# Kernel optimization log

Hardware: AMD Instinct MI355X
Metric: run time of the kernel (lower is better)

Reference implementation:

```python
import jax, jax.numpy as jnp
import numpy as np


def _cosine_alpha_bar(T, s=0.008):
    x = np.linspace(0.0, T, T + 1)
    ac = np.cos((x / T + s) / (1.0 + s) * np.pi / 2.0) ** 2
    ac = ac / ac[0]
    betas = np.clip(1.0 - ac[1:] / ac[:-1], 1e-5, 0.999)
    return jnp.asarray(np.cumprod(1.0 - betas), dtype=jnp.float32)


def setup_inputs():
    B, T, C, D, L, NS = 16, 1024, 16, 256, 4, 1000
    ks = list(jax.random.split(jax.random.key(0), 64))
    def w(i, shape, fan):
        return jax.random.normal(ks[i], shape, dtype=jnp.float32) / np.sqrt(fan)
    half = D // 2
    nf = half // 2
    inp = {}
    inp['x'] = jax.random.normal(ks[0], (B, T, C), dtype=jnp.float32)
    inp['t'] = jax.random.randint(ks[1], (B,), 0, NS, dtype=jnp.int32)
    dt = jax.random.uniform(ks[2], (B, T), minval=5e-4, maxval=2e-3, dtype=jnp.float32)
    inp['timestamps'] = jnp.cumsum(dt, axis=1)
    inp['mask'] = (jax.random.uniform(ks[3], (B, T, C)) > 0.3).astype(jnp.float32)
    inp['noise'] = jax.random.normal(ks[4], (B, T, D), dtype=jnp.float32)
    inp['n_heads'] = 4
    inp['alpha_bar'] = _cosine_alpha_bar(NS)
    inp['W_enc'] = w(5, (2 * C, D), 2 * C); inp['b_enc'] = jnp.zeros((D,), jnp.float32)
    inp['te_freqs'] = jnp.exp(-jnp.arange(half, dtype=jnp.float32) * np.log(10000.0) / half)
    inp['W_temb'] = w(6, (D, D), D); inp['b_temb'] = jnp.zeros((D,), jnp.float32)
    inp['th_a'] = 0.1 * jax.random.normal(ks[7], (half,), dtype=jnp.float32)
    inp['th_b'] = 0.1 * jax.random.normal(ks[8], (half,), dtype=jnp.float32)
    inp['th_freqs'] = (jnp.exp(-jnp.linspace(0.0, np.log(10000.0 / 4.0), nf)) * (2.0 * np.pi / 4.0)).astype(jnp.float32)
    inp['W_film'] = w(9, (D, 2 * D), D); inp['b_film'] = jnp.zeros((2 * D,), jnp.float32)
    inp['gru_Wih'] = w(10, (D, 3 * D), D); inp['gru_Whh'] = w(11, (D, 3 * D), D)
    inp['gru_bih'] = jnp.zeros((3 * D,), jnp.float32); inp['gru_bhh'] = jnp.zeros((3 * D,), jnp.float32)
    inp['ode_W1'] = w(12, (D, D), D); inp['ode_b1'] = jnp.zeros((D,), jnp.float32)
    inp['ode_W2'] = w(13, (D, D), D); inp['ode_b2'] = jnp.zeros((D,), jnp.float32)
    inp['tr_Wqkv'] = w(14, (L, D, 3 * D), D); inp['tr_bqkv'] = jnp.zeros((L, 3 * D), jnp.float32)
    inp['tr_Wo'] = w(15, (L, D, D), D); inp['tr_bo'] = jnp.zeros((L, D), jnp.float32)
    inp['tr_ln1_w'] = jnp.ones((L, D), jnp.float32); inp['tr_ln1_b'] = jnp.zeros((L, D), jnp.float32)
    inp['tr_ln2_w'] = jnp.ones((L, D), jnp.float32); inp['tr_ln2_b'] = jnp.zeros((L, D), jnp.float32)
    inp['tr_W1'] = w(16, (L, D, 4 * D), D); inp['tr_b1'] = jnp.zeros((L, 4 * D), jnp.float32)
    inp['tr_W2'] = w(17, (L, 4 * D, D), 4 * D); inp['tr_b2'] = jnp.zeros((L, D), jnp.float32)
    inp['trn_w'] = jnp.ones((D,), jnp.float32); inp['trn_b'] = jnp.zeros((D,), jnp.float32)
    return inp


def _ln(u, w_, b_):
    m = u.mean(-1, keepdims=True)
    v = u.var(-1, keepdims=True)
    return (u - m) / jnp.sqrt(v + 1e-5) * w_ + b_


def reference(x, t, timestamps, mask, noise, n_heads, alpha_bar, W_enc, b_enc, te_freqs, W_temb, b_temb, th_a, th_b, th_freqs, W_film, b_film, gru_Wih, gru_Whh, gru_bih, gru_bhh, ode_W1, ode_b1, ode_W2, ode_b2, tr_Wqkv, tr_bqkv, tr_Wo, tr_bo, tr_ln1_w, tr_ln1_b, tr_ln2_w, tr_ln2_b, tr_W1, tr_b1, tr_W2, tr_b2, trn_w, trn_b):
    B, T, C = x.shape
    D = W_enc.shape[1]
    hd = D // n_heads
    # latent encode + forward diffusion
    z = jax.nn.relu(jnp.concatenate([x, mask], -1) @ W_enc + b_enc)  # (B,T,D)
    ab = alpha_bar[t][:, None, None]
    h = jnp.sqrt(ab) * z + jnp.sqrt(1.0 - ab) * noise
    # diffusion-step sinusoidal embedding
    targ = t.astype(jnp.float32)[:, None] * te_freqs[None, :]
    te = (jnp.concatenate([jnp.sin(targ), jnp.cos(targ)], -1) @ W_temb + b_temb)[:, None, :]
    # TimeHybridEncoding: odd dims ramp, even dims interleaved sin/cos
    ts = timestamps
    ramp = ts[..., None] * th_a + th_b                       # (B,T,D/2)
    phase = ts[..., None] * th_freqs                         # (B,T,D/4)
    sc = jnp.stack([jnp.sin(phase), jnp.cos(phase)], -1).reshape(B, T, -1)
    tm = jnp.zeros((B, T, D), x.dtype).at[..., 0::2].set(sc).at[..., 1::2].set(ramp)
    gamma, beta = jnp.split(jax.nn.silu(te) @ W_film + b_film, 2, -1)
    tm = (1.0 + gamma) * tm + beta
    h = h + te + tm
    # Jump-ODE encoder: RK4 between events + GRUCell jump, as a scan
    dts = jnp.concatenate([jnp.zeros((B, 1), x.dtype), ts[:, 1:] - ts[:, :-1]], 1)[..., None]  # (B,T,1); dt0=0 -> identity ODE step
    def odef(hh):
        return jnp.tanh(hh @ ode_W1 + ode_b1) @ ode_W2 + ode_b2
    def step(hh, inp):
        xt, dt = inp
        f1 = odef(hh)
        f2 = odef(hh + 0.5 * dt * f1)
        f3 = odef(hh + 0.5 * dt * f2)
        f4 = odef(hh + dt * f3)
        hh = hh + dt / 6.0 * (f1 + 2.0 * f2 + 2.0 * f3 + f4)
        gi = xt @ gru_Wih + gru_bih
        gh = hh @ gru_Whh + gru_bhh
        ir, iz, inn = jnp.split(gi, 3, -1)
        hr, hz, hn = jnp.split(gh, 3, -1)
        r = jax.nn.sigmoid(ir + hr)
        zg = jax.nn.sigmoid(iz + hz)
        n = jnp.tanh(inn + r * hn)
        hh = (1.0 - zg) * n + zg * hh
        return hh, hh
    _, Hs = jax.lax.scan(step, jnp.zeros((B, D), x.dtype), (jnp.swapaxes(h, 0, 1), jnp.swapaxes(dts, 0, 1)))
    Hseq = jnp.swapaxes(Hs, 0, 1)  # (B,T,D)
    # pre-norm causal transformer encoder (eval mode, relu FFN), final LayerNorm
    causal = jnp.triu(jnp.full((T, T), -jnp.inf, dtype=x.dtype), 1)
    Ht = Hseq
    for l in range(tr_Wqkv.shape[0]):
        u = _ln(Ht, tr_ln1_w[l], tr_ln1_b[l])
        q, k, v = jnp.split(u @ tr_Wqkv[l] + tr_bqkv[l], 3, -1)
        q = q.reshape(B, T, n_heads, hd).transpose(0, 2, 1, 3)
        k = k.reshape(B, T, n_heads, hd).transpose(0, 2, 1, 3)
        v = v.reshape(B, T, n_heads, hd).transpose(0, 2, 1, 3)
        att = jax.nn.softmax(jnp.einsum('bhqd,bhkd->bhqk', q, k) / np.sqrt(hd) + causal, axis=-1)
        o = jnp.einsum('bhqk,bhkd->bhqd', att, v).transpose(0, 2, 1, 3).reshape(B, T, D)
        Ht = Ht + o @ tr_Wo[l] + tr_bo[l]
        u2 = _ln(Ht, tr_ln2_w[l], tr_ln2_b[l])
        Ht = Ht + jax.nn.relu(u2 @ tr_W1[l] + tr_b1[l]) @ tr_W2[l] + tr_b2[l]
    Ht = _ln(Ht, trn_w, trn_b)
    return Hseq + Ht
```

## Files before the change

### kernel.cpp

```cpp
#include <hip/hip_runtime.h>

#define Bz  16
#define Tz  1024
#define Cz  16
#define Dz  256
#define NHz 4
#define HDz 64
#define Lz  4
#define MROWS (Bz*Tz)
#define QB  8

__device__ __forceinline__ float sigmoidf_(float x){ return 1.0f/(1.0f+__expf(-x)); }
__device__ __forceinline__ float tanh_(float x){
  float e = __expf(2.f*x);
  return 1.f - 2.f/(e + 1.f);
}

__device__ __forceinline__ float dot2f(uint a, uint b, float c){
  float d;
  asm("v_dot2_f32_f16 %0, %1, %2, %3" : "=v"(d) : "v"(a), "v"(b), "v"(c));
  return d;
}
__device__ __forceinline__ uint f2h2(float a, float b){
  union { _Float16 h[2]; uint u; } r;
  r.h[0] = (_Float16)a; r.h[1] = (_Float16)b;
  return r.u;
}

__device__ __forceinline__ float red8(float a){
  int x = __builtin_amdgcn_update_dpp(0, __float_as_int(a), 0xB1, 0xF, 0xF, true);
  a += __int_as_float(x);
  x = __builtin_amdgcn_update_dpp(0, __float_as_int(a), 0x4E, 0xF, 0xF, true);
  a += __int_as_float(x);
  a += __shfl_xor(a, 4);
  return a;
}

__global__ __launch_bounds__(256) void k_prep(
    const float* __restrict__ W1, const float* __restrict__ W2, const float* __restrict__ Whh,
    uint* __restrict__ W1L, uint* __restrict__ W2L, uint* __restrict__ WhL)
{
  int m = blockIdx.x*256 + threadIdx.x;
  if (m < 65536){
    const float* W = (m < 32768) ? W1 : W2;
    uint* out = (m < 32768) ? W1L : W2L;
    int mm = m & 32767;
    int q = mm >> 2, cc = mm & 3;
    int i = q >> 9, l = q & 511;
    int j4 = l >> 3, ks = l & 7;
    int kp = ks*16 + i;
    int c = j4*4 + cc;
    out[mm] = f2h2(W[(2*kp)*256 + c], W[(2*kp+1)*256 + c]);
  } else if (m < 65536 + 98304){
    int mm = m - 65536;
    int g = mm >> 15;
    int r = mm & 32767;
    int q = r >> 2, cc = r & 3;
    int i = q >> 9, l = q & 511;
    int j4 = l >> 3, ks = l & 7;
    int kp = ks*16 + i;
    int c = j4*4 + cc;
    WhL[mm] = f2h2(Whh[(2*kp)*768 + g*256 + c], Whh[(2*kp+1)*768 + g*256 + c]);
  }
}

__global__ __launch_bounds__(256) void k_batch_emb(
    const int* __restrict__ t, const float* __restrict__ te_freqs,
    const float* __restrict__ W_temb, const float* __restrict__ b_temb,
    const float* __restrict__ W_film, const float* __restrict__ b_film,
    float* __restrict__ te_out, float* __restrict__ gamma_out, float* __restrict__ beta_out)
{
  int b = blockIdx.x; int j = threadIdx.x;
  __shared__ float s[256];
  __shared__ float ste[256];
  float tf = (float)t[b];
  if (j < 128){
    float targ = tf * te_freqs[j];
    s[j]     = __sinf(targ);
    s[j+128] = __cosf(targ);
  }
  __syncthreads();
  float a0=0,a1=0,a2=0,a3=0;
  #pragma unroll 8
  for (int k=0;k<256;k+=4){
    a0 = fmaf(s[k+0], W_temb[(k+0)*256+j], a0);
    a1 = fmaf(s[k+1], W_temb[(k+1)*256+j], a1);
    a2 = fmaf(s[k+2], W_temb[(k+2)*256+j], a2);
    a3 = fmaf(s[k+3], W_temb[(k+3)*256+j], a3);
  }
  float te = (a0+a1)+(a2+a3) + b_temb[j];
  te_out[b*256+j] = te;
  ste[j] = te * sigmoidf_(te);
  __syncthreads();
  float g0=0,g1=0,h0=0,h1=0;
  #pragma unroll 8
  for (int k=0;k<256;k+=2){
    float v0 = ste[k+0], v1 = ste[k+1];
    g0 = fmaf(v0, W_film[(k+0)*512+j],     g0);
    g1 = fmaf(v1, W_film[(k+1)*512+j],     g1);
    h0 = fmaf(v0, W_film[(k+0)*512+256+j], h0);
    h1 = fmaf(v1, W_film[(k+1)*512+256+j], h1);
  }
  gamma_out[b*256+j] = g0+g1 + b_film[j];
  beta_out [b*256+j] = h0+h1 + b_film[256+j];
}

__global__ __launch_bounds__(256) void k_encode(
    const float* __restrict__ x, const float* __restrict__ mask, const float* __restrict__ noise,
    const int* __restrict__ t, const float* __restrict__ alpha_bar, const float* __restrict__ ts,
    const float* __restrict__ W_enc, const float* __restrict__ b_enc,
    const float* __restrict__ th_a, const float* __restrict__ th_b, const float* __restrict__ th_freqs,
    const float* __restrict__ te, const float* __restrict__ gamma, const float* __restrict__ beta,
    float* __restrict__ H0)
{
  int bt = blockIdx.x; int b = bt >> 10;
  int j = threadIdx.x;
  __shared__ float in[32];
  if (j < 16)      in[j] = x[bt*16 + j];
  else if (j < 32) in[j] = mask[bt*16 + (j-16)];
  __syncthreads();
  float acc = 0.f;
  #pragma unroll
  for (int k=0;k<32;k++) acc = fmaf(in[k], W_enc[k*256+j], acc);
  float z = fmaxf(acc + b_enc[j], 0.f);
  float ab = alpha_bar[t[b]];
  float h = sqrtf(ab)*z + sqrtf(1.f-ab)*noise[(size_t)bt*256 + j];
  float tsv = ts[bt];
  float tm;
  if (j & 1){
    int i = (j-1) >> 1;
    tm = fmaf(tsv, th_a[i], th_b[i]);
  } else {
    int m = j >> 2;
    float ph = tsv * th_freqs[m];
    tm = ((j & 3) == 0) ? __sinf(ph) : __cosf(ph);
  }
  tm = fmaf(1.f + gamma[b*256+j], tm, beta[b*256+j]);
  H0[(size_t)bt*256 + j] = h + te[b*256+j] + tm;
}

template<bool RELU, bool RES>
__global__ __launch_bounds__(256) void k_gemm(
    const float* __restrict__ A, const float* __restrict__ W,
    const float* __restrict__ bias, const float* __restrict__ Rp,
    float* __restrict__ Cp, int M, int N, int K)
{
  __shared__ float As[16][68];
  __shared__ float Bs[16][64];
  int bn = blockIdx.x * 64, bm = blockIdx.y * 64;
  int tid = threadIdx.x;
  int tx = tid & 15, ty = tid >> 4;
  float acc[4][4] = {};
  for (int k0=0; k0<K; k0+=16){
    #pragma unroll
    for (int i=0;i<4;i++){
      int idx = tid + i*256;
      int m = idx >> 4, kk = idx & 15;
      As[kk][m] = A[(size_t)(bm+m)*K + k0+kk];
    }
    #pragma unroll
    for (int i=0;i<4;i++){
      int idx = tid + i*256;
      int kk = idx >> 6, n = idx & 63;
      Bs[kk][n] = W[(size_t)(k0+kk)*N + bn+n];
    }
    __syncthreads();
    #pragma unroll
    for (int kk=0;kk<16;kk++){
      float a0=As[kk][ty*4+0], a1=As[kk][ty*4+1], a2=As[kk][ty*4+2], a3=As[kk][ty*4+3];
      float b0=Bs[kk][tx*4+0], b1=Bs[kk][tx*4+1], b2=Bs[kk][tx*4+2], b3=Bs[kk][tx*4+3];
      acc[0][0]=fmaf(a0,b0,acc[0][0]); acc[0][1]=fmaf(a0,b1,acc[0][1]); acc[0][2]=fmaf(a0,b2,acc[0][2]); acc[0][3]=fmaf(a0,b3,acc[0][3]);
      acc[1][0]=fmaf(a1,b0,acc[1][0]); acc[1][1]=fmaf(a1,b1,acc[1][1]); acc[1][2]=fmaf(a1,b2,acc[1][2]); acc[1][3]=fmaf(a1,b3,acc[1][3]);
      acc[2][0]=fmaf(a2,b0,acc[2][0]); acc[2][1]=fmaf(a2,b1,acc[2][1]); acc[2][2]=fmaf(a2,b2,acc[2][2]); acc[2][3]=fmaf(a2,b3,acc[2][3]);
      acc[3][0]=fmaf(a3,b0,acc[3][0]); acc[3][1]=fmaf(a3,b1,acc[3][1]); acc[3][2]=fmaf(a3,b2,acc[3][2]); acc[3][3]=fmaf(a3,b3,acc[3][3]);
    }
    __syncthreads();
  }
  #pragma unroll
  for (int i=0;i<4;i++){
    int row = bm + ty*4 + i;
    #pragma unroll
    for (int jj=0;jj<4;jj++){
      int col = bn + tx*4 + jj;
      float v = acc[i][jj] + bias[col];
      if (RELU) v = fmaxf(v, 0.f);
      if (RES)  v += Rp[(size_t)row*N + col];
      Cp[(size_t)row*N + col] = v;
    }
  }
}

#define SCAN_LDS_BYTES (131072 + 1280)

#define DOT4V(WV, VW) { uint4 _w = (WV); \
  a0 = dot2f(_w.x, VW, a0); a1 = dot2f(_w.y, VW, a1); \
  a2 = dot2f(_w.z, VW, a2); a3 = dot2f(_w.w, VW, a3); }

#define MV16L(VB) { \
  uint4 q0=(VB)[ks5+0], q1=(VB)[ks5+1], q2=(VB)[ks5+2], q3=(VB)[ks5+3]; \
  DOT4V(w1s[0*512+tid], q0.x)  DOT4V(w1s[1*512+tid], q0.y)  DOT4V(w1s[2*512+tid], q0.z)  DOT4V(w1s[3*512+tid], q0.w)  \
  DOT4V(w1s[4*512+tid], q1.x)  DOT4V(w1s[5*512+tid], q1.y)  DOT4V(w1s[6*512+tid], q1.z)  DOT4V(w1s[7*512+tid], q1.w)  \
  DOT4V(w1s[8*512+tid], q2.x)  DOT4V(w1s[9*512+tid], q2.y)  DOT4V(w1s[10*512+tid], q2.z) DOT4V(w1s[11*512+tid], q2.w) \
  DOT4V(w1s[12*512+tid], q3.x) DOT4V(w1s[13*512+tid], q3.y) DOT4V(w1s[14*512+tid], q3.z) DOT4V(w1s[15*512+tid], q3.w) }

#define MV16R(W, VB) { \
  uint4 q0=(VB)[ks5+0], q1=(VB)[ks5+1], q2=(VB)[ks5+2], q3=(VB)[ks5+3]; \
  DOT4V(W[0], q0.x)  DOT4V(W[1], q0.y)  DOT4V(W[2], q0.z)  DOT4V(W[3], q0.w)  \
  DOT4V(W[4], q1.x)  DOT4V(W[5], q1.y)  DOT4V(W[6], q1.z)  DOT4V(W[7], q1.w)  \
  DOT4V(W[8], q2.x)  DOT4V(W[9], q2.y)  DOT4V(W[10], q2.z) DOT4V(W[11], q2.w) \
  DOT4V(W[12], q3.x) DOT4V(W[13], q3.y) DOT4V(W[14], q3.z) DOT4V(W[15], q3.w) }

#define DOTG(WV, VV, g0,g1,g2,g3) \
  g0 = dot2f((WV).x, VV, g0); g1 = dot2f((WV).y, VV, g1); \
  g2 = dot2f((WV).z, VV, g2); g3 = dot2f((WV).w, VV, g3);

#define LDQ(BUF, PO, I0) { \
  BUF[0]=WhL4[(PO)+((I0)+0)*512+tid]; BUF[1]=WhL4[(PO)+((I0)+1)*512+tid]; \
  BUF[2]=WhL4[(PO)+((I0)+2)*512+tid]; BUF[3]=WhL4[(PO)+((I0)+3)*512+tid]; }

#define DOTQ(BUF, Q, g0,g1,g2,g3) { \
  DOTG(BUF[0], (Q).x, g0,g1,g2,g3) DOTG(BUF[1], (Q).y, g0,g1,g2,g3) \
  DOTG(BUF[2], (Q).z, g0,g1,g2,g3) DOTG(BUF[3], (Q).w, g0,g1,g2,g3) }

__global__ __launch_bounds__(512, 2) void k_scan(
    const uint* __restrict__ W1Lg, const uint* __restrict__ W2Lg, const uint* __restrict__ WhLg,
    const float* __restrict__ GI, const float* __restrict__ ts,
    const float* __restrict__ b1, const float* __restrict__ b2,
    const float* __restrict__ bhh, float* __restrict__ Hseq, float* __restrict__ Ht)
{
  extern __shared__ __align__(16) char smem[];
  uint4* w1s = (uint4*)smem;
  uint*  v2  = (uint*)(smem + 131072);
  const int b = blockIdx.x, tid = threadIdx.x;
  const int j4 = tid >> 3, ks = tid & 7;
  const int ks5 = ks*5;
  const uint4* W1L4 = (const uint4*)W1Lg;
  const uint4* W2L4 = (const uint4*)W2Lg;
  const uint4* WhL4 = (const uint4*)WhLg;
  #pragma unroll
  for (int i=0;i<16;i++) w1s[i*512+tid] = W1L4[i*512+tid];
  uint4 w2r[16];
  #pragma unroll
  for (int i=0;i<16;i++) w2r[i] = W2L4[i*512 + tid];
  if (tid < 320) v2[tid] = 0u;
  const float4 b1v  = ((const float4*)b1)[j4];
  const float4 b2v  = ((const float4*)b2)[j4];
  const float4 bhrv = ((const float4*)bhh)[j4];
  const float4 bhzv = ((const float4*)bhh)[64 + j4];
  const float4 bhnv = ((const float4*)bhh)[128 + j4];
  const float* tsb = ts + b*Tz;
  const float* gib = GI + (size_t)b*Tz*768;
  float* hsq = Hseq + (size_t)b*Tz*256;
  float* htp = Ht   + (size_t)b*Tz*256;
  const int wdw = 2*j4;
  const int wslot = (wdw >> 4)*20 + (wdw & 15);
  float4 h = {0.f,0.f,0.f,0.f};
  float tprev = 0.f;
  int cur = 0;
  __syncthreads();

  for (int tt=0; tt<Tz; ++tt){
    float tcur = tsb[tt];
    float dt = tcur - tprev; if (tt == 0) dt = 0.f;
    tprev = tcur;
    uint* bufA = v2 + (cur ? 160 : 0);
    uint* bufB = v2 + (cur ? 0 : 160);
    const uint4* vbA = (const uint4*)bufA;
    const uint4* vbB = (const uint4*)bufB;
    uint4 wA[4], wB[4];

    {
      float a0=0,a1=0,a2=0,a3=0;
      MV16L(vbA);
      a0=red8(a0); a1=red8(a1); a2=red8(a2); a3=red8(a3);
      float u0 = tanh_(a0+b1v.x), u1 = tanh_(a1+b1v.y);
      float u2 = tanh_(a2+b1v.z), u3 = tanh_(a3+b1v.w);
      if (ks == 0){
        uint2 pk; pk.x = f2h2(u0,u1); pk.y = f2h2(u2,u3);
        *(uint2*)(bufB + wslot) = pk;
      }
    }
    __syncthreads();
    {
      float a0=0,a1=0,a2=0,a3=0;
      MV16R(w2r, vbB);
      a0=red8(a0); a1=red8(a1); a2=red8(a2); a3=red8(a3);
      float hm = 0.5f*dt;
      float m0 = fmaf(hm, a0+b2v.x, h.x);
      float m1 = fmaf(hm, a1+b2v.y, h.y);
      float m2 = fmaf(hm, a2+b2v.z, h.z);
      float m3 = fmaf(hm, a3+b2v.w, h.w);
      if (ks == 0){
        uint2 pk; pk.x = f2h2(m0,m1); pk.y = f2h2(m2,m3);
        *(uint2*)(bufA + wslot) = pk;
      }
    }
    __syncthreads();
    {
      float a0=0,a1=0,a2=0,a3=0;
      MV16L(vbA);
      a0=red8(a0); a1=red8(a1); a2=red8(a2); a3=red8(a3);
      float u0 = tanh_(a0+b1v.x), u1 = tanh_(a1+b1v.y);
      float u2 = tanh_(a2+b1v.z), u3 = tanh_(a3+b1v.w);
      if (ks == 0){
        uint2 pk; pk.x = f2h2(u0,u1); pk.y = f2h2(u2,u3);
        *(uint2*)(bufB + wslot) = pk;
      }
    }
    __syncthreads();
    float4 hn;
    const float4 gi_r = *(const float4*)(gib + tt*768       + j4*4);
    const float4 gi_z = *(const float4*)(gib + tt*768 + 256 + j4*4);
    const float4 gi_n = *(const float4*)(gib + tt*768 + 512 + j4*4);
    LDQ(wA, 0, 0)
    LDQ(wB, 0, 4)
    {
      float a0=0,a1=0,a2=0,a3=0;
      MV16R(w2r, vbB);
      a0=red8(a0); a1=red8(a1); a2=red8(a2); a3=red8(a3);
      hn.x = fmaf(dt, a0+b2v.x, h.x);
      hn.y = fmaf(dt, a1+b2v.y, h.y);
      hn.z = fmaf(dt, a2+b2v.z, h.z);
      hn.w = fmaf(dt, a3+b2v.w, h.w);
      if (ks == 0){
        uint2 pk; pk.x = f2h2(hn.x,hn.y); pk.y = f2h2(hn.z,hn.w);
        *(uint2*)(bufA + wslot) = pk;
      }
    }
    __syncthreads();
    {
      uint4 q0=vbA[ks5+0], q1=vbA[ks5+1], q2=vbA[ks5+2], q3=vbA[ks5+3];
      float r0=0,r1=0,r2=0,r3=0, z0=0,z1=0,z2=0,z3=0, n0=0,n1=0,n2=0,n3=0;
      DOTQ(wA, q0, r0,r1,r2,r3)  LDQ(wA, 0, 8)
      DOTQ(wB, q1, r0,r1,r2,r3)  LDQ(wB, 0, 12)
      DOTQ(wA, q2, r0,r1,r2,r3)  LDQ(wA, 8192, 0)
      DOTQ(wB, q3, r0,r1,r2,r3)  LDQ(wB, 8192, 4)
      DOTQ(wA, q0, z0,z1,z2,z3)  LDQ(wA, 8192, 8)
      DOTQ(wB, q1, z0,z1,z2,z3)  LDQ(wB, 8192, 12)
      DOTQ(wA, q2, z0,z1,z2,z3)  LDQ(wA, 16384, 0)
      DOTQ(wB, q3, z0,z1,z2,z3)  LDQ(wB, 16384, 4)
      DOTQ(wA, q0, n0,n1,n2,n3)  LDQ(wA, 16384, 8)
      DOTQ(wB, q1, n0,n1,n2,n3)  LDQ(wB, 16384, 12)
      DOTQ(wA, q2, n0,n1,n2,n3)
      DOTQ(wB, q3, n0,n1,n2,n3)
      r0=red8(r0); r1=red8(r1); r2=red8(r2); r3=red8(r3);
      z0=red8(z0); z1=red8(z1); z2=red8(z2); z3=red8(z3);
      n0=red8(n0); n1=red8(n1); n2=red8(n2); n3=red8(n3);
      float gr0 = sigmoidf_(gi_r.x + r0 + bhrv.x);
      float gr1 = sigmoidf_(gi_r.y + r1 + bhrv.y);
      float gr2 = sigmoidf_(gi_r.z + r2 + bhrv.z);
      float gr3 = sigmoidf_(gi_r.w + r3 + bhrv.w);
      float gz0 = sigmoidf_(gi_z.x + z0 + bhzv.x);
      float gz1 = sigmoidf_(gi_z.y + z1 + bhzv.y);
      float gz2 = sigmoidf_(gi_z.z + z2 + bhzv.z);
      float gz3 = sigmoidf_(gi_z.w + z3 + bhzv.w);
      float gn0 = tanh_(gi_n.x + gr0*(n0 + bhnv.x));
      float gn1 = tanh_(gi_n.y + gr1*(n1 + bhnv.y));
      float gn2 = tanh_(gi_n.z + gr2*(n2 + bhnv.z));
      float gn3 = tanh_(gi_n.w + gr3*(n3 + bhnv.w));
      h.x = fmaf(gz0, hn.x - gn0, gn0);
      h.y = fmaf(gz1, hn.y - gn1, gn1);
      h.z = fmaf(gz2, hn.z - gn2, gn2);
      h.w = fmaf(gz3, hn.w - gn3, gn3);
      if (ks == 0){
        uint2 pk; pk.x = f2h2(h.x,h.y); pk.y = f2h2(h.z,h.w);
        *(uint2*)(bufB + wslot) = pk;
        *(float4*)(hsq + tt*256 + j4*4) = h;
        *(float4*)(htp + tt*256 + j4*4) = h;
      }
    }
    cur ^= 1;
    __syncthreads();
  }
}

__global__ __launch_bounds__(256) void k_attn(const float* __restrict__ QKV, float* __restrict__ O)
{
  int qb = blockIdx.x & (Tz/QB - 1);
  int bh = blockIdx.x / (Tz/QB);
  int b = bh >> 2, h = bh & 3;
  __shared__ uint Q2[QB][32];
  __shared__ float S[QB][Tz];
  __shared__ __align__(16) char kvbuf[64*68*4];
  __shared__ float rs[QB];
  uint  (*K2)[33] = (uint(*)[33])kvbuf;
  float (*Vs)[68] = (float(*)[68])kvbuf;
  int tid = threadIdx.x;
  const float* base = QKV + (size_t)b*Tz*768;
  for (int i = tid; i < QB*16; i += 256){
    int q = i >> 4, c = i & 15;
    const float4 v = *(const float4*)&base[(size_t)(qb*QB+q)*768 + h*64 + c*4];
    Q2[q][c*2]   = f2h2(v.x*0.125f, v.y*0.125f);
    Q2[q][c*2+1] = f2h2(v.z*0.125f, v.w*0.125f);
  }
  __syncthreads();
  int kmax = qb*QB + QB;
  int nkt = (kmax + 63) >> 6;
  int q = tid >> 5, i0 = tid & 31;
  int qg = qb*QB + q;
  for (int kt=0; kt<nkt; ++kt){
    for (int i=tid; i<64*16; i+=256){
      int r=i>>4, c=i&15;
      const float4 v = *(const float4*)&base[(size_t)(kt*64+r)*768 + 256 + h*64 + c*4];
      K2[r][c*2]   = f2h2(v.x, v.y);
      K2[r][c*2+1] = f2h2(v.z, v.w);
    }
    __syncthreads();
    float a0=0.f, a1=0.f;
    #pragma unroll 8
    for (int dp=0; dp<32; ++dp){
      uint qv = Q2[q][dp];
      a0 = dot2f(K2[i0][dp],    qv, a0);
      a1 = dot2f(K2[i0+32][dp], qv, a1);
    }
    int k0g = kt*64 + i0, k1g = k0g + 32;
    S[q][kt*64+i0]    = (k0g <= qg) ? a0 : -1e30f;
    S[q][kt*64+i0+32] = (k1g <= qg) ? a1 : -1e30f;
    __syncthreads();
  }
  int NK = nkt*64;
  float m = -1e30f;
  for (int kk=i0; kk<NK; kk+=32) m = fmaxf(m, S[q][kk]);
  #pragma unroll
  for (int o=16;o;o>>=1) m = fmaxf(m, __shfl_xor(m, o, 32));
  float sum = 0.f;
  for (int kk=i0; kk<NK; kk+=32){
    float p = __expf(S[q][kk] - m);
    S[q][kk] = p;
    sum += p;
  }
  #pragma unroll
  for (int o=16;o;o>>=1) sum += __shfl_xor(sum, o, 32);
  if (i0 == 0) rs[q] = 1.f/sum;
  int dq = tid & 15;
  int ks = (tid >> 4) & 1;
  float o0=0,o1=0,o2=0,o3=0;
  for (int kt=0; kt<nkt; ++kt){
    __syncthreads();
    for (int i=tid; i<64*16; i+=256){
      int r=i>>4, c=i&15;
      const float4 v = *(const float4*)&base[(size_t)(kt*64+r)*768 + 512 + h*64 + c*4];
      *(float4*)&Vs[r][c*4] = v;
    }
    __syncthreads();
    int kbase = kt*64;
    #pragma unroll 8
    for (int kk=ks; kk<64; kk+=2){
      float p = S[q][kbase+kk];
      const float4 vv = *(const float4*)&Vs[kk][dq*4];
      o0=fmaf(p,vv.x,o0); o1=fmaf(p,vv.y,o1); o2=fmaf(p,vv.z,o2); o3=fmaf(p,vv.w,o3);
    }
  }
  o0 += __shfl_xor(o0, 16); o1 += __shfl_xor(o1, 16);
  o2 += __shfl_xor(o2, 16); o3 += __shfl_xor(o3, 16);
  if (!(tid & 16)){
    float r = rs[q];
    size_t orow = ((size_t)b*Tz + qg)*256 + h*64 + dq*4;
    float4 ov = {o0*r, o1*r, o2*r, o3*r};
    *(float4*)&O[orow] = ov;
  }
}

template<bool FINAL>
__global__ __launch_bounds__(256) void k_ln(
    const float* __restrict__ in, const float* __restrict__ w, const float* __restrict__ bgain,
    const float* __restrict__ addv, float* __restrict__ out)
{
  int row  = blockIdx.x*4 + (threadIdx.x >> 6);
  int lane = threadIdx.x & 63;
  const float4 xv = ((const float4*)(in + (size_t)row*256))[lane];
  float s = xv.x + xv.y + xv.z + xv.w;
  #pragma unroll
  for (int o=32;o;o>>=1) s += __shfl_xor(s, o, 64);
  float mean = s * (1.f/256.f);
  float dx=xv.x-mean, dy=xv.y-mean, dz=xv.z-mean, dw=xv.w-mean;
  float qv = dx*dx + dy*dy + dz*dz + dw*dw;
  #pragma unroll
  for (int o=32;o;o>>=1) qv += __shfl_xor(qv, o, 64);
  float rstd = 1.f/sqrtf(qv*(1.f/256.f) + 1e-5f);
  const float4 wv = ((const float4*)w)[lane];
  const float4 bv = ((const float4*)bgain)[lane];
  float4 ov;
  ov.x = dx*rstd*wv.x + bv.x;
  ov.y = dy*rstd*wv.y + bv.y;
  ov.z = dz*rstd*wv.z + bv.z;
  ov.w = dw*rstd*wv.w + bv.w;
  if (FINAL){
    const float4 av = ((const float4*)(addv + (size_t)row*256))[lane];
    ov.x += av.x; ov.y += av.y; ov.z += av.z; ov.w += av.w;
  }
  ((float4*)(out + (size_t)row*256))[lane] = ov;
}

extern "C" void kernel_launch(void* const* d_in, const int* in_sizes, int n_in,
                              void* d_out, int out_size, void* d_ws, size_t ws_size,
                              hipStream_t stream)
{
  const float* x         = (const float*)d_in[0];
  const int*   t         = (const int*)  d_in[1];
  const float* ts        = (const float*)d_in[2];
  const float* mask      = (const float*)d_in[3];
  const float* noise     = (const float*)d_in[4];
  const float* alpha_bar = (const float*)d_in[6];
  const float* W_enc     = (const float*)d_in[7];
  const float* b_enc     = (const float*)d_in[8];
  const float* te_freqs  = (const float*)d_in[9];
  const float* W_temb    = (const float*)d_in[10];
  const float* b_temb    = (const float*)d_in[11];
  const float* th_a      = (const float*)d_in[12];
  const float* th_b      = (const float*)d_in[13];
  const float* th_freqs  = (const float*)d_in[14];
  const float* W_film    = (const float*)d_in[15];
  const float* b_film    = (const float*)d_in[16];
  const float* gru_Wih   = (const float*)d_in[17];
  const float* gru_Whh   = (const float*)d_in[18];
  const float* gru_bih   = (const float*)d_in[19];
  const float* gru_bhh   = (const float*)d_in[20];
  const float* ode_W1    = (const float*)d_in[21];
  const float* ode_b1    = (const float*)d_in[22];
  const float* ode_W2    = (const float*)d_in[23];
  const float* ode_b2    = (const float*)d_in[24];
  const float* tr_Wqkv   = (const float*)d_in[25];
  const float* tr_bqkv   = (const float*)d_in[26];
  const float* tr_Wo     = (const float*)d_in[27];
  const float* tr_bo     = (const float*)d_in[28];
  const float* tr_ln1_w  = (const float*)d_in[29];
  const float* tr_ln1_b  = (const float*)d_in[30];
  const float* tr_ln2_w  = (const float*)d_in[31];
  const float* tr_ln2_b  = (const float*)d_in[32];
  const float* tr_W1     = (const float*)d_in[33];
  const float* tr_b1     = (const float*)d_in[34];
  const float* tr_W2     = (const float*)d_in[35];
  const float* tr_b2     = (const float*)d_in[36];
  const float* trn_w     = (const float*)d_in[37];
  const float* trn_b     = (const float*)d_in[38];

  float* w = (float*)d_ws;
  float* te    = w;
  float* gamma = w + 4096;
  float* beta  = w + 8192;
  float* R1    = w + 12288;
  float* H0    = R1;
  float* GI    = R1 + 4*1024*1024;
  float* QKVb  = R1;
  float* F1    = R1;
  float* Hseq  = R1   + 16*1024*1024;
  float* Ht    = Hseq + 4*1024*1024;
  float* U     = Ht   + 4*1024*1024;
  float* O     = U    + 4*1024*1024;
  uint*  W1L   = (uint*)(O + 4*1024*1024);
  uint*  W2L   = W1L + 32768;
  uint*  WhL   = W2L + 32768;

  k_prep<<<640, 256, 0, stream>>>(ode_W1, ode_W2, gru_Whh, W1L, W2L, WhL);
  k_batch_emb<<<Bz, 256, 0, stream>>>(t, te_freqs, W_temb, b_temb, W_film, b_film, te, gamma, beta);
  k_encode<<<MROWS, 256, 0, stream>>>(x, mask, noise, t, alpha_bar, ts, W_enc, b_enc,
                                      th_a, th_b, th_freqs, te, gamma, beta, H0);
  k_gemm<false,false><<<dim3(768/64, MROWS/64), 256, 0, stream>>>(H0, gru_Wih, gru_bih, nullptr, GI, MROWS, 768, 256);

  hipFuncSetAttribute((const void*)k_scan, hipFuncAttributeMaxDynamicSharedMemorySize, SCAN_LDS_BYTES);
  k_scan<<<Bz, 512, SCAN_LDS_BYTES, stream>>>(W1L, W2L, WhL, GI, ts, ode_b1, ode_b2, gru_bhh, Hseq, Ht);

  for (int l=0; l<Lz; ++l){
    k_ln<false><<<MROWS/4, 256, 0, stream>>>(Ht, tr_ln1_w + l*256, tr_ln1_b + l*256, nullptr, U);
    k_gemm<false,false><<<dim3(768/64, MROWS/64), 256, 0, stream>>>(U, tr_Wqkv + (size_t)l*256*768, tr_bqkv + l*768, nullptr, QKVb, MROWS, 768, 256);
    k_attn<<<Bz*NHz*(Tz/QB), 256, 0, stream>>>(QKVb, O);
    k_gemm<false,true><<<dim3(256/64, MROWS/64), 256, 0, stream>>>(O, tr_Wo + (size_t)l*256*256, tr_bo + l*256, Ht, Ht, MROWS, 256, 256);
    k_ln<false><<<MROWS/4, 256, 0, stream>>>(Ht, tr_ln2_w + l*256, tr_ln2_b + l*256, nullptr, U);
    k_gemm<true,false><<<dim3(1024/64, MROWS/64), 256, 0, stream>>>(U, tr_W1 + (size_t)l*256*1024, tr_b1 + l*1024, nullptr, F1, MROWS, 1024, 256);
    k_gemm<false,true><<<dim3(256/64, MROWS/64), 256, 0, stream>>>(F1, tr_W2 + (size_t)l*1024*256, tr_b2 + l*256, Ht, Ht, MROWS, 256, 1024);
  }

  k_ln<true><<<MROWS/4, 256, 0, stream>>>(Ht, trn_w, trn_b, Hseq, (float*)d_out);
}
```

Measured before the change: 12.93 ms.

## Double scan block to 1024 threads with 16-way K split per output

The sequential GRU/ODE scan kernel now runs 1024 threads per batch block instead of 512. Each group of four outputs is split across 16 K-slices rather than 8, which halves the per-thread dot-product chain, register weight footprint and global Whh loads per step. The weight prep layout, LDS vector padding and reductions (one more cross-lane shuffle) are adjusted to match. This trades shorter serial per-step latency for more reduction overhead and a larger synchronization domain at each barrier.

```diff
diff --git a/kernel.cpp b/kernel.cpp
--- a/kernel.cpp
+++ b/kernel.cpp
@@ -27,12 +27,13 @@
   return r.u;
 }
 
-__device__ __forceinline__ float red8(float a){
+__device__ __forceinline__ float red16(float a){
   int x = __builtin_amdgcn_update_dpp(0, __float_as_int(a), 0xB1, 0xF, 0xF, true);
   a += __int_as_float(x);
   x = __builtin_amdgcn_update_dpp(0, __float_as_int(a), 0x4E, 0xF, 0xF, true);
   a += __int_as_float(x);
   a += __shfl_xor(a, 4);
+  a += __shfl_xor(a, 8);
   return a;
 }
 
@@ -46,20 +47,20 @@
     uint* out = (m < 32768) ? W1L : W2L;
     int mm = m & 32767;
     int q = mm >> 2, cc = mm & 3;
-    int i = q >> 9, l = q & 511;
-    int j4 = l >> 3, ks = l & 7;
-    int kp = ks*16 + i;
-    int c = j4*4 + cc;
+    int i = q >> 10, l = q & 1023;
+    int ks = l & 15, j4g = l >> 4;
+    int kp = ks*8 + i;
+    int c = j4g*4 + cc;
     out[mm] = f2h2(W[(2*kp)*256 + c], W[(2*kp+1)*256 + c]);
   } else if (m < 65536 + 98304){
     int mm = m - 65536;
     int g = mm >> 15;
     int r = mm & 32767;
     int q = r >> 2, cc = r & 3;
-    int i = q >> 9, l = q & 511;
-    int j4 = l >> 3, ks = l & 7;
-    int kp = ks*16 + i;
-    int c = j4*4 + cc;
+    int i = q >> 10, l = q & 1023;
+    int ks = l & 15, j4g = l >> 4;
+    int kp = ks*8 + i;
+    int c = j4g*4 + cc;
     WhL[mm] = f2h2(Whh[(2*kp)*768 + g*256 + c], Whh[(2*kp+1)*768 + g*256 + c]);
   }
 }
@@ -190,39 +191,33 @@
   }
 }
 
-#define SCAN_LDS_BYTES (131072 + 1280)
+#define SCAN_LDS_BYTES (131072 + 1536)
 
 #define DOT4V(WV, VW) { uint4 _w = (WV); \
   a0 = dot2f(_w.x, VW, a0); a1 = dot2f(_w.y, VW, a1); \
   a2 = dot2f(_w.z, VW, a2); a3 = dot2f(_w.w, VW, a3); }
 
-#define MV16L(VB) { \
-  uint4 q0=(VB)[ks5+0], q1=(VB)[ks5+1], q2=(VB)[ks5+2], q3=(VB)[ks5+3]; \
-  DOT4V(w1s[0*512+tid], q0.x)  DOT4V(w1s[1*512+tid], q0.y)  DOT4V(w1s[2*512+tid], q0.z)  DOT4V(w1s[3*512+tid], q0.w)  \
-  DOT4V(w1s[4*512+tid], q1.x)  DOT4V(w1s[5*512+tid], q1.y)  DOT4V(w1s[6*512+tid], q1.z)  DOT4V(w1s[7*512+tid], q1.w)  \
-  DOT4V(w1s[8*512+tid], q2.x)  DOT4V(w1s[9*512+tid], q2.y)  DOT4V(w1s[10*512+tid], q2.z) DOT4V(w1s[11*512+tid], q2.w) \
-  DOT4V(w1s[12*512+tid], q3.x) DOT4V(w1s[13*512+tid], q3.y) DOT4V(w1s[14*512+tid], q3.z) DOT4V(w1s[15*512+tid], q3.w) }
-
-#define MV16R(W, VB) { \
-  uint4 q0=(VB)[ks5+0], q1=(VB)[ks5+1], q2=(VB)[ks5+2], q3=(VB)[ks5+3]; \
-  DOT4V(W[0], q0.x)  DOT4V(W[1], q0.y)  DOT4V(W[2], q0.z)  DOT4V(W[3], q0.w)  \
-  DOT4V(W[4], q1.x)  DOT4V(W[5], q1.y)  DOT4V(W[6], q1.z)  DOT4V(W[7], q1.w)  \
-  DOT4V(W[8], q2.x)  DOT4V(W[9], q2.y)  DOT4V(W[10], q2.z) DOT4V(W[11], q2.w) \
-  DOT4V(W[12], q3.x) DOT4V(W[13], q3.y) DOT4V(W[14], q3.z) DOT4V(W[15], q3.w) }
+#define MV8L(VB) { \
+  uint4 p0=(VB)[ks3+0], p1=(VB)[ks3+1]; \
+  DOT4V(w1s[0*1024+tid],p0.x) DOT4V(w1s[1*1024+tid],p0.y) \
+  DOT4V(w1s[2*1024+tid],p0.z) DOT4V(w1s[3*1024+tid],p0.w) \
+  DOT4V(w1s[4*1024+tid],p1.x) DOT4V(w1s[5*1024+tid],p1.y) \
+  DOT4V(w1s[6*1024+tid],p1.z) DOT4V(w1s[7*1024+tid],p1.w) }
+
+#define MV8R(W, VB) { \
+  uint4 p0=(VB)[ks3+0], p1=(VB)[ks3+1]; \
+  DOT4V(W[0],p0.x) DOT4V(W[1],p0.y) DOT4V(W[2],p0.z) DOT4V(W[3],p0.w) \
+  DOT4V(W[4],p1.x) DOT4V(W[5],p1.y) DOT4V(W[6],p1.z) DOT4V(W[7],p1.w) }
 
 #define DOTG(WV, VV, g0,g1,g2,g3) \
   g0 = dot2f((WV).x, VV, g0); g1 = dot2f((WV).y, VV, g1); \
   g2 = dot2f((WV).z, VV, g2); g3 = dot2f((WV).w, VV, g3);
 
-#define LDQ(BUF, PO, I0) { \
-  BUF[0]=WhL4[(PO)+((I0)+0)*512+tid]; BUF[1]=WhL4[(PO)+((I0)+1)*512+tid]; \
-  BUF[2]=WhL4[(PO)+((I0)+2)*512+tid]; BUF[3]=WhL4[(PO)+((I0)+3)*512+tid]; }
-
-#define DOTQ(BUF, Q, g0,g1,g2,g3) { \
-  DOTG(BUF[0], (Q).x, g0,g1,g2,g3) DOTG(BUF[1], (Q).y, g0,g1,g2,g3) \
-  DOTG(BUF[2], (Q).z, g0,g1,g2,g3) DOTG(BUF[3], (Q).w, g0,g1,g2,g3) }
-
-__global__ __launch_bounds__(512, 2) void k_scan(
+#define LDQ4(BUF, PO, I0) { \
+  BUF[0]=WhL4[(PO)+((I0)+0)*1024+tid]; BUF[1]=WhL4[(PO)+((I0)+1)*1024+tid]; \
+  BUF[2]=WhL4[(PO)+((I0)+2)*1024+tid]; BUF[3]=WhL4[(PO)+((I0)+3)*1024+tid]; }
+
+__global__ __launch_bounds__(1024, 4) void k_scan(
     const uint* __restrict__ W1Lg, const uint* __restrict__ W2Lg, const uint* __restrict__ WhLg,
     const float* __restrict__ GI, const float* __restrict__ ts,
     const float* __restrict__ b1, const float* __restrict__ b2,
@@ -232,17 +227,17 @@
   uint4* w1s = (uint4*)smem;
   uint*  v2  = (uint*)(smem + 131072);
   const int b = blockIdx.x, tid = threadIdx.x;
-  const int j4 = tid >> 3, ks = tid & 7;
-  const int ks5 = ks*5;
+  const int j4 = tid >> 4, ks = tid & 15;
+  const int ks3 = ks*3;
   const uint4* W1L4 = (const uint4*)W1Lg;
   const uint4* W2L4 = (const uint4*)W2Lg;
   const uint4* WhL4 = (const uint4*)WhLg;
   #pragma unroll
-  for (int i=0;i<16;i++) w1s[i*512+tid] = W1L4[i*512+tid];
-  uint4 w2r[16];
-  #pragma unroll
-  for (int i=0;i<16;i++) w2r[i] = W2L4[i*512 + tid];
-  if (tid < 320) v2[tid] = 0u;
+  for (int i=0;i<8;i++) w1s[i*1024+tid] = W1L4[i*1024+tid];
+  uint4 w2r[8];
+  #pragma unroll
+  for (int i=0;i<8;i++) w2r[i] = W2L4[i*1024 + tid];
+  if (tid < 384) v2[tid] = 0u;
   const float4 b1v  = ((const float4*)b1)[j4];
   const float4 b2v  = ((const float4*)b2)[j4];
   const float4 bhrv = ((const float4*)bhh)[j4];
@@ -253,7 +248,7 @@
   float* hsq = Hseq + (size_t)b*Tz*256;
   float* htp = Ht   + (size_t)b*Tz*256;
   const int wdw = 2*j4;
-  const int wslot = (wdw >> 4)*20 + (wdw & 15);
+  const int wslot = (wdw >> 3)*12 + (wdw & 7);
   float4 h = {0.f,0.f,0.f,0.f};
   float tprev = 0.f;
   int cur = 0;
@@ -263,16 +258,16 @@
     float tcur = tsb[tt];
     float dt = tcur - tprev; if (tt == 0) dt = 0.f;
     tprev = tcur;
-    uint* bufA = v2 + (cur ? 160 : 0);
-    uint* bufB = v2 + (cur ? 0 : 160);
+    uint* bufA = v2 + (cur ? 192 : 0);
+    uint* bufB = v2 + (cur ? 0 : 192);
     const uint4* vbA = (const uint4*)bufA;
     const uint4* vbB = (const uint4*)bufB;
     uint4 wA[4], wB[4];
 
     {
       float a0=0,a1=0,a2=0,a3=0;
-      MV16L(vbA);
-      a0=red8(a0); a1=red8(a1); a2=red8(a2); a3=red8(a3);
+      MV8L(vbA);
+      a0=red16(a0); a1=red16(a1); a2=red16(a2); a3=red16(a3);
       float u0 = tanh_(a0+b1v.x), u1 = tanh_(a1+b1v.y);
       float u2 = tanh_(a2+b1v.z), u3 = tanh_(a3+b1v.w);
       if (ks == 0){
@@ -283,8 +278,8 @@
     __syncthreads();
     {
       float a0=0,a1=0,a2=0,a3=0;
-      MV16R(w2r, vbB);
-      a0=red8(a0); a1=red8(a1); a2=red8(a2); a3=red8(a3);
+      MV8R(w2r, vbB);
+      a0=red16(a0); a1=red16(a1); a2=red16(a2); a3=red16(a3);
       float hm = 0.5f*dt;
       float m0 = fmaf(hm, a0+b2v.x, h.x);
       float m1 = fmaf(hm, a1+b2v.y, h.y);
@@ -298,8 +293,8 @@
     __syncthreads();
     {
       float a0=0,a1=0,a2=0,a3=0;
-      MV16L(vbA);
-      a0=red8(a0); a1=red8(a1); a2=red8(a2); a3=red8(a3);
+      MV8L(vbA);
+      a0=red16(a0); a1=red16(a1); a2=red16(a2); a3=red16(a3);
       float u0 = tanh_(a0+b1v.x), u1 = tanh_(a1+b1v.y);
       float u2 = tanh_(a2+b1v.z), u3 = tanh_(a3+b1v.w);
       if (ks == 0){
@@ -312,12 +307,12 @@
     const float4 gi_r = *(const float4*)(gib + tt*768       + j4*4);
     const float4 gi_z = *(const float4*)(gib + tt*768 + 256 + j4*4);
     const float4 gi_n = *(const float4*)(gib + tt*768 + 512 + j4*4);
-    LDQ(wA, 0, 0)
-    LDQ(wB, 0, 4)
+    LDQ4(wA, 0, 0)
+    LDQ4(wB, 0, 4)
     {
       float a0=0,a1=0,a2=0,a3=0;
-      MV16R(w2r, vbB);
-      a0=red8(a0); a1=red8(a1); a2=red8(a2); a3=red8(a3);
+      MV8R(w2r, vbB);
+      a0=red16(a0); a1=red16(a1); a2=red16(a2); a3=red16(a3);
       hn.x = fmaf(dt, a0+b2v.x, h.x);
       hn.y = fmaf(dt, a1+b2v.y, h.y);
       hn.z = fmaf(dt, a2+b2v.z, h.z);
@@ -329,23 +324,27 @@
     }
     __syncthreads();
     {
-      uint4 q0=vbA[ks5+0], q1=vbA[ks5+1], q2=vbA[ks5+2], q3=vbA[ks5+3];
+      uint4 p0=vbA[ks3+0], p1=vbA[ks3+1];
       float r0=0,r1=0,r2=0,r3=0, z0=0,z1=0,z2=0,z3=0, n0=0,n1=0,n2=0,n3=0;
-      DOTQ(wA, q0, r0,r1,r2,r3)  LDQ(wA, 0, 8)
-      DOTQ(wB, q1, r0,r1,r2,r3)  LDQ(wB, 0, 12)
-      DOTQ(wA, q2, r0,r1,r2,r3)  LDQ(wA, 8192, 0)
-      DOTQ(wB, q3, r0,r1,r2,r3)  LDQ(wB, 8192, 4)
-      DOTQ(wA, q0, z0,z1,z2,z3)  LDQ(wA, 8192, 8)
-      DOTQ(wB, q1, z0,z1,z2,z3)  LDQ(wB, 8192, 12)
-      DOTQ(wA, q2, z0,z1,z2,z3)  LDQ(wA, 16384, 0)
-      DOTQ(wB, q3, z0,z1,z2,z3)  LDQ(wB, 16384, 4)
-      DOTQ(wA, q0, n0,n1,n2,n3)  LDQ(wA, 16384, 8)
-      DOTQ(wB, q1, n0,n1,n2,n3)  LDQ(wB, 16384, 12)
-      DOTQ(wA, q2, n0,n1,n2,n3)
-      DOTQ(wB, q3, n0,n1,n2,n3)
-      r0=red8(r0); r1=red8(r1); r2=red8(r2); r3=red8(r3);
-      z0=red8(z0); z1=red8(z1); z2=red8(z2); z3=red8(z3);
-      n0=red8(n0); n1=red8(n1); n2=red8(n2); n3=red8(n3);
+      DOTG(wA[0],p0.x, r0,r1,r2,r3) DOTG(wA[1],p0.y, r0,r1,r2,r3)
+      DOTG(wA[2],p0.z, r0,r1,r2,r3) DOTG(wA[3],p0.w, r0,r1,r2,r3)
+      LDQ4(wA, 8192, 0)
+      DOTG(wB[0],p1.x, r0,r1,r2,r3) DOTG(wB[1],p1.y, r0,r1,r2,r3)
+      DOTG(wB[2],p1.z, r0,r1,r2,r3) DOTG(wB[3],p1.w, r0,r1,r2,r3)
+      LDQ4(wB, 8192, 4)
+      DOTG(wA[0],p0.x, z0,z1,z2,z3) DOTG(wA[1],p0.y, z0,z1,z2,z3)
+      DOTG(wA[2],p0.z, z0,z1,z2,z3) DOTG(wA[3],p0.w, z0,z1,z2,z3)
+      LDQ4(wA, 16384, 0)
+      DOTG(wB[0],p1.x, z0,z1,z2,z3) DOTG(wB[1],p1.y, z0,z1,z2,z3)
+      DOTG(wB[2],p1.z, z0,z1,z2,z3) DOTG(wB[3],p1.w, z0,z1,z2,z3)
+      LDQ4(wB, 16384, 4)
+      DOTG(wA[0],p0.x, n0,n1,n2,n3) DOTG(wA[1],p0.y, n0,n1,n2,n3)
+      DOTG(wA[2],p0.z, n0,n1,n2,n3) DOTG(wA[3],p0.w, n0,n1,n2,n3)
+      DOTG(wB[0],p1.x, n0,n1,n2,n3) DOTG(wB[1],p1.y, n0,n1,n2,n3)
+      DOTG(wB[2],p1.z, n0,n1,n2,n3) DOTG(wB[3],p1.w, n0,n1,n2,n3)
+      r0=red16(r0); r1=red16(r1); r2=red16(r2); r3=red16(r3);
+      z0=red16(z0); z1=red16(z1); z2=red16(z2); z3=red16(z3);
+      n0=red16(n0); n1=red16(n1); n2=red16(n2); n3=red16(n3);
       float gr0 = sigmoidf_(gi_r.x + r0 + bhrv.x);
       float gr1 = sigmoidf_(gi_r.y + r1 + bhrv.y);
       float gr2 = sigmoidf_(gi_r.z + r2 + bhrv.z);
@@ -559,7 +558,7 @@
   k_gemm<false,false><<<dim3(768/64, MROWS/64), 256, 0, stream>>>(H0, gru_Wih, gru_bih, nullptr, GI, MROWS, 768, 256);
 
   hipFuncSetAttribute((const void*)k_scan, hipFuncAttributeMaxDynamicSharedMemorySize, SCAN_LDS_BYTES);
-  k_scan<<<Bz, 512, SCAN_LDS_BYTES, stream>>>(W1L, W2L, WhL, GI, ts, ode_b1, ode_b2, gru_bhh, Hseq, Ht);
+  k_scan<<<Bz, 1024, SCAN_LDS_BYTES, stream>>>(W1L, W2L, WhL, GI, ts, ode_b1, ode_b2, gru_bhh, Hseq, Ht);
 
   for (int l=0; l<Lz; ++l){
     k_ln<false><<<MROWS/4, 256, 0, stream>>>(Ht, tr_ln1_w + l*256, tr_ln1_b + l*256, nullptr, U);
```

Measured after the change: 20.11 ms. +55.5%, slower.
